# Optimization experiments

Hardware: AMD Instinct MI355X
Metric: run time of the kernel (lower is better)

## Reference

```python
import jax, jax.numpy as jnp
import numpy as np

B, T, C, H, D = 4, 1024, 1024, 16, 64  # batch, seq, n_embd, heads, head_size


def setup_inputs() -> dict:
    key = jax.random.key(0)
    ks = jax.random.split(key, 6)
    x = jax.random.normal(ks[0], (B, T, C), dtype=jnp.float32)
    s = 0.02
    Wq = jax.random.normal(ks[1], (H, C, D), dtype=jnp.float32) * s
    Wk = jax.random.normal(ks[2], (H, C, D), dtype=jnp.float32) * s
    Wv = jax.random.normal(ks[3], (H, C, D), dtype=jnp.float32) * s
    Wo = jax.random.normal(ks[4], (H * D, C), dtype=jnp.float32) * s
    bo = jnp.zeros((C,), dtype=jnp.float32)
    return {"x": x, "Wq": Wq, "Wk": Wk, "Wv": Wv, "Wo": Wo, "bo": bo}


def reference(x, Wq, Wk, Wv, Wo, bo):
    # per-head projections (bias=False Linears), all heads batched via einsum
    q = jnp.einsum("btc,hcd->bhtd", x, Wq)
    k = jnp.einsum("btc,hcd->bhtd", x, Wk)
    v = jnp.einsum("btc,hcd->bhtd", x, Wv)
    # scaled dot-product scores: [B,H,T,T]
    scale = 1.0 / jnp.sqrt(jnp.asarray(D, dtype=q.dtype))
    scores = jnp.einsum("bhtd,bhsd->bhts", q, k) * scale
    # causal mask (tril), masked_fill with -inf equivalent
    causal = jnp.tril(jnp.ones((T, T), dtype=bool))
    neg = jnp.finfo(scores.dtype).min
    scores = jnp.where(causal[None, None], scores, neg)
    att = jax.nn.softmax(scores, axis=-1)
    # weighted aggregation of values, then concat heads
    out = jnp.einsum("bhts,bhsd->bhtd", att, v)
    out = out.transpose(0, 2, 1, 3).reshape(B, T, H * D)
    # output projection
    return out @ Wo + bo
```

## Files before the change

### kernel.cpp

```cpp
#include <hip/hip_runtime.h>
#include <hip/hip_bf16.h>
#include <stdint.h>


typedef float f32x4 __attribute__((ext_vector_type(4)));
typedef __bf16 bf16x8 __attribute__((ext_vector_type(8)));
typedef __bf16 bf16x4 __attribute__((ext_vector_type(4)));

#define GAS __attribute__((address_space(1)))
#define LAS __attribute__((address_space(3)))

__global__ __launch_bounds__(256) void cast_bf16_kernel(
    const float* __restrict__ in, __bf16* __restrict__ out, int n4) {
  int i = blockIdx.x * 256 + threadIdx.x;
  if (i < n4) {
    float4 f = ((const float4*)in)[i];
    bf16x4 o;
    o[0] = (__bf16)f.x; o[1] = (__bf16)f.y; o[2] = (__bf16)f.z; o[3] = (__bf16)f.w;
    ((bf16x4*)out)[i] = o;
  }
}

__global__ __launch_bounds__(256) void transpose_qkv_kernel(
    const float* __restrict__ Wq, const float* __restrict__ Wk,
    const float* __restrict__ Wv, __bf16* __restrict__ dst_base) {
  __shared__ float tile[64][65];
  int z = blockIdx.z;
  const float* s = (z < 16 ? Wq : (z < 32 ? Wk : Wv)) + (size_t)(z & 15) * 65536;
  __bf16* d = dst_base + (size_t)z * 65536;
  int r0 = blockIdx.x * 64;
  int tx = threadIdx.x & 63, ty = threadIdx.x >> 6;
#pragma unroll
  for (int rr = ty; rr < 64; rr += 4)
    tile[rr][tx] = s[(size_t)(r0 + rr) * 64 + tx];
  __syncthreads();
#pragma unroll
  for (int rr = ty; rr < 64; rr += 4)
    d[(size_t)rr * 1024 + (r0 + tx)] = (__bf16)tile[tx][rr];
}

__global__ __launch_bounds__(256) void transpose_cast_kernel(
    const float* __restrict__ src, __bf16* __restrict__ dst,
    int src_ld, int dst_ld) {
  __shared__ float tile[64][65];
  int r0 = blockIdx.x * 64, c0 = blockIdx.y * 64;
  int tx = threadIdx.x & 63, ty = threadIdx.x >> 6;
#pragma unroll
  for (int rr = ty; rr < 64; rr += 4)
    tile[rr][tx] = src[(size_t)(r0 + rr) * src_ld + (c0 + tx)];
  __syncthreads();
#pragma unroll
  for (int rr = ty; rr < 64; rr += 4)
    dst[(size_t)(c0 + rr) * dst_ld + (r0 + tx)] = (__bf16)tile[tx][rr];
}

template <int MODE>
__global__ __launch_bounds__(256) void gemm_bt_kernel(
    const __bf16* __restrict__ A, const __bf16* __restrict__ BT, int N,
    __bf16* __restrict__ qo, __bf16* __restrict__ ko, __bf16* __restrict__ vo,
    float* __restrict__ Cout, const float* __restrict__ bias) {
  constexpr int K = 1024;
  extern __shared__ __align__(16) char smem_raw[];
  __bf16* Ash = (__bf16*)smem_raw;
  __bf16* Bsh = Ash + 2 * 128 * 32;
  const int tid = threadIdx.x;
  const int wid = tid >> 6, lane = tid & 63;
  const int fr = lane & 15, fq = lane >> 4;
  const int m0 = blockIdx.x * 128, n0 = blockIdx.y * 128;
  const int wr = wid >> 1, wc = wid & 1;
  const int srow = lane >> 2;
  const int scol = (((lane & 3) ^ ((lane >> 3) & 3))) * 8;
  const int swz = ((fq ^ ((fr >> 1) & 3))) << 3;

  f32x4 acc[4][4] = {};

  auto stage = [&](int k0, int buf) {
#pragma unroll
    for (int i = 0; i < 2; ++i) {
      int chunk = wid * 2 + i;
      int row = chunk * 16 + srow;
      const __bf16* gA = A + (size_t)(m0 + row) * K + k0 + scol;
      const __bf16* gB = BT + (size_t)(n0 + row) * K + k0 + scol;
      __builtin_amdgcn_global_load_lds((const GAS void*)gA, (LAS void*)&Ash[buf * 4096 + chunk * 512], 16, 0, 0);
      __builtin_amdgcn_global_load_lds((const GAS void*)gB, (LAS void*)&Bsh[buf * 4096 + chunk * 512], 16, 0, 0);
    }
  };

  stage(0, 0);
  __syncthreads();
  int buf = 0;
  for (int k0 = 0; k0 < K; k0 += 32) {
    if (k0 + 32 < K) stage(k0 + 32, buf ^ 1);
    bf16x8 af[4], bfr[4];
#pragma unroll
    for (int mi = 0; mi < 4; ++mi) {
      int r = wr * 64 + mi * 16 + fr;
      af[mi] = *(const bf16x8*)&Ash[buf * 4096 + r * 32 + swz];
    }
#pragma unroll
    for (int ni = 0; ni < 4; ++ni) {
      int r = wc * 64 + ni * 16 + fr;
      bfr[ni] = *(const bf16x8*)&Bsh[buf * 4096 + r * 32 + swz];
    }
    __builtin_amdgcn_s_setprio(1);
#pragma unroll
    for (int mi = 0; mi < 4; ++mi)
#pragma unroll
      for (int ni = 0; ni < 4; ++ni)
        acc[mi][ni] = __builtin_amdgcn_mfma_f32_16x16x32_bf16(af[mi], bfr[ni], acc[mi][ni], 0, 0, 0);
    __builtin_amdgcn_s_setprio(0);
    __syncthreads();
    buf ^= 1;
  }

  if (MODE == 0 && (n0 >> 10) == 2) {
    __bf16* spill = (__bf16*)smem_raw;
#pragma unroll
    for (int mi = 0; mi < 4; ++mi)
#pragma unroll
      for (int ni = 0; ni < 4; ++ni) {
        int nl = wc * 64 + ni * 16 + fr;
        int ml = wr * 64 + mi * 16 + fq * 4;
        bf16x4 pk;
#pragma unroll
        for (int r = 0; r < 4; ++r) pk[r] = (__bf16)acc[mi][ni][r];
        *(bf16x4*)&spill[nl * 136 + ml] = pk;
      }
    __syncthreads();
    const int b = m0 >> 10, t0 = m0 & 1023;
    const int lrow = lane >> 4, lch = lane & 15;
#pragma unroll
    for (int i = 0; i < 8; ++i) {
      int nl = wid * 32 + i * 4 + lrow;
      bf16x8 v = *(const bf16x8*)&spill[nl * 136 + lch * 8];
      int nn = (n0 & 1023) + nl;
      *(bf16x8*)&vo[(((size_t)b * 16 + (nn >> 6)) * 64 + (nn & 63)) * 1024 + t0 + lch * 8] = v;
    }
    return;
  }

#pragma unroll
  for (int mi = 0; mi < 4; ++mi) {
#pragma unroll
    for (int ni = 0; ni < 4; ++ni) {
      int n = n0 + wc * 64 + ni * 16 + fr;
      int mb = m0 + wr * 64 + mi * 16 + fq * 4;
#pragma unroll
      for (int r = 0; r < 4; ++r) {
        int m = mb + r;
        float val = acc[mi][ni][r];
        if (MODE == 0) {
          int sec = n >> 10, nl = n & 1023;
          int h = nl >> 6, dd = nl & 63;
          int b = m >> 10, t = m & 1023;
          if (sec == 0) {
            qo[(((size_t)b * 16 + h) * 1024 + t) * 64 + dd] = (__bf16)(val * 0.125f);
          } else {
            ko[(((size_t)b * 16 + h) * 1024 + t) * 64 + dd] = (__bf16)val;
          }
        } else {
          Cout[(size_t)m * N + n] = val + bias[n];
        }
      }
    }
  }
}

__global__ __launch_bounds__(256) void attn_fwd_kernel(
    const __bf16* __restrict__ Q, const __bf16* __restrict__ Kg,
    const __bf16* __restrict__ Vt, __bf16* __restrict__ O) {
  __shared__ __align__(16) __bf16 Ksh[2][64 * 64];
  __shared__ __align__(16) __bf16 VTs[2][64 * 64];
  __shared__ __align__(16) __bf16 Psh[4][16 * 72];

  const int bid = blockIdx.x;
  const int bx = (bid >> 3) & 7;
  const int bh = (bid & 7) | ((bid >> 6) << 3);
  const int b = bh >> 4, h = bh & 15;
  const size_t base = (size_t)bh * 1024 * 64;
  const int tid = threadIdx.x, wid = tid >> 6, lane = tid & 63;
  const int fr = lane & 15, fq = lane >> 4;
  const int qta = bx, qtb = 15 - bx;
  const int q0a = qta * 64, q0b = qtb * 64;

  bf16x8 qa[2], qbf[2];
  {
    int qra = q0a + wid * 16 + fr;
    qa[0] = *(const bf16x8*)&Q[base + (size_t)qra * 64 + fq * 8];
    qa[1] = *(const bf16x8*)&Q[base + (size_t)qra * 64 + 32 + fq * 8];
    int qrb = q0b + wid * 16 + fr;
    qbf[0] = *(const bf16x8*)&Q[base + (size_t)qrb * 64 + fq * 8];
    qbf[1] = *(const bf16x8*)&Q[base + (size_t)qrb * 64 + 32 + fq * 8];
  }
  f32x4 oa[4] = {}, ob[4] = {};
  float ma = -1e30f, la = 0.f, mb = -1e30f, lb = 0.f;

  const int lrow8 = lane >> 3;
  const int schunk = (lane & 7) ^ lrow8;

  auto stage = [&](int st, int buf) {
    const int s0 = st * 64;
#pragma unroll
    for (int i = 0; i < 2; ++i) {
      int rowbase = i * 32 + wid * 8;
      int row = rowbase + lrow8;
      const __bf16* gK = Kg + base + (size_t)(s0 + row) * 64 + schunk * 8;
      __builtin_amdgcn_global_load_lds((const GAS void*)gK,
          (LAS void*)&Ksh[buf][rowbase * 64], 16, 0, 0);
      const __bf16* gV = Vt + base + (size_t)row * 1024 + s0 + schunk * 8;
      __builtin_amdgcn_global_load_lds((const GAS void*)gV,
          (LAS void*)&VTs[buf][rowbase * 64], 16, 0, 0);
    }
  };

  auto compute = [&](int buf, int s0, const bf16x8* qf, f32x4* oacc,
                     float& m, float& l, int q0x, bool maskT) {
    f32x4 s[4];
    __builtin_amdgcn_s_setprio(1);
#pragma unroll
    for (int sf = 0; sf < 4; ++sf) {
      int row = sf * 16 + fr, rx = fr & 7;
      bf16x8 kf0 = *(const bf16x8*)&Ksh[buf][row * 64 + ((fq ^ rx) << 3)];
      f32x4 z = {};
      s[sf] = __builtin_amdgcn_mfma_f32_16x16x32_bf16(kf0, qf[0], z, 0, 0, 0);
      bf16x8 kf1 = *(const bf16x8*)&Ksh[buf][row * 64 + (((4 + fq) ^ rx) << 3)];
      s[sf] = __builtin_amdgcn_mfma_f32_16x16x32_bf16(kf1, qf[1], s[sf], 0, 0, 0);
    }
    __builtin_amdgcn_s_setprio(0);

    const int qg = q0x + wid * 16 + fr;
    float sv[4][4];
    float mx = -1e30f;
#pragma unroll
    for (int sf = 0; sf < 4; ++sf)
#pragma unroll
      for (int r = 0; r < 4; ++r) {
        float x = s[sf][r];
        if (maskT) { int sg = s0 + sf * 16 + fq * 4 + r; if (sg > qg) x = -1e30f; }
        sv[sf][r] = x;
        mx = fmaxf(mx, x);
      }
    mx = fmaxf(mx, __shfl_xor(mx, 16));
    mx = fmaxf(mx, __shfl_xor(mx, 32));
    float mnew = fmaxf(m, mx);
    float alpha = __expf(m - mnew);
    m = mnew;
    float rs = 0.f;
#pragma unroll
    for (int sf = 0; sf < 4; ++sf) {
      bf16x4 pk;
#pragma unroll
      for (int r = 0; r < 4; ++r) {
        float p = __expf(sv[sf][r] - mnew);
        rs += p;
        pk[r] = (__bf16)p;
      }
      *(bf16x4*)&Psh[wid][fr * 72 + sf * 16 + fq * 4] = pk;
    }
    rs += __shfl_xor(rs, 16);
    rs += __shfl_xor(rs, 32);
    l = l * alpha + rs;
    float ar[4];
#pragma unroll
    for (int r = 0; r < 4; ++r) ar[r] = __shfl(alpha, (lane & 48) | (fq * 4 + r));
#pragma unroll
    for (int df = 0; df < 4; ++df)
#pragma unroll
      for (int r = 0; r < 4; ++r) oacc[df][r] *= ar[r];

    __builtin_amdgcn_s_setprio(1);
#pragma unroll
    for (int kk = 0; kk < 2; ++kk) {
      bf16x8 pf = *(const bf16x8*)&Psh[wid][fr * 72 + kk * 32 + fq * 8];
#pragma unroll
      for (int df = 0; df < 4; ++df) {
        int row = df * 16 + fr;
        bf16x8 vf = *(const bf16x8*)&VTs[buf][row * 64 + ((((kk << 2) | fq) ^ (fr & 7)) << 3)];
        oacc[df] = __builtin_amdgcn_mfma_f32_16x16x32_bf16(pf, vf, oacc[df], 0, 0, 0);
      }
    }
    __builtin_amdgcn_s_setprio(0);
  };

  stage(0, 0);
  __syncthreads();
  int cur = 0;
  for (int st = 0; st <= qtb; ++st) {
    if (st < qtb) stage(st + 1, cur ^ 1);
    compute(cur, st * 64, qbf, ob, mb, lb, q0b, st == qtb);
    if (st <= qta) compute(cur, st * 64, qa, oa, ma, la, q0a, st == qta);
    __syncthreads();
    cur ^= 1;
  }

  auto epilogue = [&](const f32x4* oacc, float l, int q0x) {
    float lr[4];
#pragma unroll
    for (int r = 0; r < 4; ++r) lr[r] = __shfl(l, (lane & 48) | (fq * 4 + r));
#pragma unroll
    for (int r = 0; r < 4; ++r) {
      float inv = 1.0f / lr[r];
      int t = q0x + wid * 16 + fq * 4 + r;
      size_t orow = ((size_t)b * 1024 + t) * 1024 + h * 64;
#pragma unroll
      for (int df = 0; df < 4; ++df)
        O[orow + df * 16 + fr] = (__bf16)(oacc[df][r] * inv);
    }
  };
  epilogue(ob, lb, q0b);
  epilogue(oa, la, q0a);
}

extern "C" void kernel_launch(void* const* d_in, const int* in_sizes, int n_in,
                              void* d_out, int out_size, void* d_ws, size_t ws_size,
                              hipStream_t stream) {
  const float* x  = (const float*)d_in[0];
  const float* Wq = (const float*)d_in[1];
  const float* Wk = (const float*)d_in[2];
  const float* Wv = (const float*)d_in[3];
  const float* Wo = (const float*)d_in[4];
  const float* bo = (const float*)d_in[5];
  float* out = (float*)d_out;

  __bf16* xb    = (__bf16*)d_ws;
  __bf16* wqkvT = xb + (size_t)4096 * 1024;
  __bf16* woT   = wqkvT + (size_t)3072 * 1024;
  __bf16* qb    = woT + (size_t)1024 * 1024;
  __bf16* kb    = qb + (size_t)4 * 16 * 1024 * 64;
  __bf16* vtb   = kb + (size_t)4 * 16 * 1024 * 64;
  __bf16* Ob    = vtb + (size_t)4 * 16 * 1024 * 64;

  cast_bf16_kernel<<<4096, 256, 0, stream>>>(x, xb, 4194304 / 4);
  transpose_qkv_kernel<<<dim3(16, 1, 48), 256, 0, stream>>>(Wq, Wk, Wv, wqkvT);
  transpose_cast_kernel<<<dim3(16, 16), 256, 0, stream>>>(Wo, woT, 1024, 1024);

  gemm_bt_kernel<0><<<dim3(32, 24), 256, 34816, stream>>>(xb, wqkvT, 3072, qb, kb, vtb, nullptr, nullptr);

  attn_fwd_kernel<<<512, 256, 0, stream>>>(qb, kb, vtb, Ob);

  gemm_bt_kernel<1><<<dim3(32, 8), 256, 32768, stream>>>(Ob, woT, 1024, nullptr, nullptr, nullptr, out, bo);
}
```

Measured before the change: 102.3 us.

## Split paired causal q-tiles into separate blocks and add lazy softmax rescaling

The attention kernel no longer pairs a short and a long causal query tile in one block. It launches 1024 blocks of one q-tile each, ordered longest-first, to double parallelism and let the scheduler balance the work. It also skips the running-max update and accumulator rescale unless some lane's new max exceeds the old one by more than 8, which removes exp, shuffle and multiply work on most iterations. Each block reloads its K/V tiles without sharing them between two q-tiles, and the lazy threshold lets exponentials grow up to e^8 before they are renormalized, which stays within fp32/bf16 range.

```diff
diff --git a/kernel.cpp b/kernel.cpp
--- a/kernel.cpp
+++ b/kernel.cpp
@@ -150,10 +150,10 @@
         int m = mb + r;
         float val = acc[mi][ni][r];
         if (MODE == 0) {
-          int sec = n >> 10, nl = n & 1023;
+          int nl = n & 1023;
           int h = nl >> 6, dd = nl & 63;
           int b = m >> 10, t = m & 1023;
-          if (sec == 0) {
+          if ((n >> 10) == 0) {
             qo[(((size_t)b * 16 + h) * 1024 + t) * 64 + dd] = (__bf16)(val * 0.125f);
           } else {
             ko[(((size_t)b * 16 + h) * 1024 + t) * 64 + dd] = (__bf16)val;
@@ -174,26 +174,22 @@
   __shared__ __align__(16) __bf16 Psh[4][16 * 72];
 
   const int bid = blockIdx.x;
-  const int bx = (bid >> 3) & 7;
-  const int bh = (bid & 7) | ((bid >> 6) << 3);
+  const int qt = 15 - (bid >> 6);
+  const int bh = bid & 63;
   const int b = bh >> 4, h = bh & 15;
   const size_t base = (size_t)bh * 1024 * 64;
   const int tid = threadIdx.x, wid = tid >> 6, lane = tid & 63;
   const int fr = lane & 15, fq = lane >> 4;
-  const int qta = bx, qtb = 15 - bx;
-  const int q0a = qta * 64, q0b = qtb * 64;
-
-  bf16x8 qa[2], qbf[2];
+  const int q0 = qt * 64;
+
+  bf16x8 qf[2];
   {
-    int qra = q0a + wid * 16 + fr;
-    qa[0] = *(const bf16x8*)&Q[base + (size_t)qra * 64 + fq * 8];
-    qa[1] = *(const bf16x8*)&Q[base + (size_t)qra * 64 + 32 + fq * 8];
-    int qrb = q0b + wid * 16 + fr;
-    qbf[0] = *(const bf16x8*)&Q[base + (size_t)qrb * 64 + fq * 8];
-    qbf[1] = *(const bf16x8*)&Q[base + (size_t)qrb * 64 + 32 + fq * 8];
-  }
-  f32x4 oa[4] = {}, ob[4] = {};
-  float ma = -1e30f, la = 0.f, mb = -1e30f, lb = 0.f;
+    int qr = q0 + wid * 16 + fr;
+    qf[0] = *(const bf16x8*)&Q[base + (size_t)qr * 64 + fq * 8];
+    qf[1] = *(const bf16x8*)&Q[base + (size_t)qr * 64 + 32 + fq * 8];
+  }
+  f32x4 oacc[4] = {};
+  float m = -1e30f, l = 0.f;
 
   const int lrow8 = lane >> 3;
   const int schunk = (lane & 7) ^ lrow8;
@@ -213,8 +209,7 @@
     }
   };
 
-  auto compute = [&](int buf, int s0, const bf16x8* qf, f32x4* oacc,
-                     float& m, float& l, int q0x, bool maskT) {
+  auto compute = [&](int buf, int s0, bool maskT) {
     f32x4 s[4];
     __builtin_amdgcn_s_setprio(1);
 #pragma unroll
@@ -228,7 +223,7 @@
     }
     __builtin_amdgcn_s_setprio(0);
 
-    const int qg = q0x + wid * 16 + fr;
+    const int qg = q0 + wid * 16 + fr;
     float sv[4][4];
     float mx = -1e30f;
 #pragma unroll
@@ -242,16 +237,26 @@
       }
     mx = fmaxf(mx, __shfl_xor(mx, 16));
     mx = fmaxf(mx, __shfl_xor(mx, 32));
-    float mnew = fmaxf(m, mx);
-    float alpha = __expf(m - mnew);
-    m = mnew;
+    if (__any(mx - m > 8.0f)) {
+      float mnew = fmaxf(m, mx);
+      float alpha = __expf(m - mnew);
+      m = mnew;
+      l *= alpha;
+      float ar[4];
+#pragma unroll
+      for (int r = 0; r < 4; ++r) ar[r] = __shfl(alpha, (lane & 48) | (fq * 4 + r));
+#pragma unroll
+      for (int df = 0; df < 4; ++df)
+#pragma unroll
+        for (int r = 0; r < 4; ++r) oacc[df][r] *= ar[r];
+    }
     float rs = 0.f;
 #pragma unroll
     for (int sf = 0; sf < 4; ++sf) {
       bf16x4 pk;
 #pragma unroll
       for (int r = 0; r < 4; ++r) {
-        float p = __expf(sv[sf][r] - mnew);
+        float p = __expf(sv[sf][r] - m);
         rs += p;
         pk[r] = (__bf16)p;
       }
@@ -259,14 +264,7 @@
     }
     rs += __shfl_xor(rs, 16);
     rs += __shfl_xor(rs, 32);
-    l = l * alpha + rs;
-    float ar[4];
-#pragma unroll
-    for (int r = 0; r < 4; ++r) ar[r] = __shfl(alpha, (lane & 48) | (fq * 4 + r));
-#pragma unroll
-    for (int df = 0; df < 4; ++df)
-#pragma unroll
-      for (int r = 0; r < 4; ++r) oacc[df][r] *= ar[r];
+    l += rs;
 
     __builtin_amdgcn_s_setprio(1);
 #pragma unroll
@@ -285,30 +283,25 @@
   stage(0, 0);
   __syncthreads();
   int cur = 0;
-  for (int st = 0; st <= qtb; ++st) {
-    if (st < qtb) stage(st + 1, cur ^ 1);
-    compute(cur, st * 64, qbf, ob, mb, lb, q0b, st == qtb);
-    if (st <= qta) compute(cur, st * 64, qa, oa, ma, la, q0a, st == qta);
+  for (int st = 0; st <= qt; ++st) {
+    if (st < qt) stage(st + 1, cur ^ 1);
+    compute(cur, st * 64, st == qt);
     __syncthreads();
     cur ^= 1;
   }
 
-  auto epilogue = [&](const f32x4* oacc, float l, int q0x) {
-    float lr[4];
-#pragma unroll
-    for (int r = 0; r < 4; ++r) lr[r] = __shfl(l, (lane & 48) | (fq * 4 + r));
-#pragma unroll
-    for (int r = 0; r < 4; ++r) {
-      float inv = 1.0f / lr[r];
-      int t = q0x + wid * 16 + fq * 4 + r;
-      size_t orow = ((size_t)b * 1024 + t) * 1024 + h * 64;
-#pragma unroll
-      for (int df = 0; df < 4; ++df)
-        O[orow + df * 16 + fr] = (__bf16)(oacc[df][r] * inv);
-    }
-  };
-  epilogue(ob, lb, q0b);
-  epilogue(oa, la, q0a);
+  float lr[4];
+#pragma unroll
+  for (int r = 0; r < 4; ++r) lr[r] = __shfl(l, (lane & 48) | (fq * 4 + r));
+#pragma unroll
+  for (int r = 0; r < 4; ++r) {
+    float inv = 1.0f / lr[r];
+    int t = q0 + wid * 16 + fq * 4 + r;
+    size_t orow = ((size_t)b * 1024 + t) * 1024 + h * 64;
+#pragma unroll
+    for (int df = 0; df < 4; ++df)
+      O[orow + df * 16 + fr] = (__bf16)(oacc[df][r] * inv);
+  }
 }
 
 extern "C" void kernel_launch(void* const* d_in, const int* in_sizes, int n_in,
@@ -336,7 +329,8 @@
 
   gemm_bt_kernel<0><<<dim3(32, 24), 256, 34816, stream>>>(xb, wqkvT, 3072, qb, kb, vtb, nullptr, nullptr);
 
-  attn_fwd_kernel<<<512, 256, 0, stream>>>(qb, kb, vtb, Ob);
-
-  gemm_bt_kernel<1><<<dim3(32, 8), 256, 32768, stream>>>(Ob, woT, 1024, nullptr, nullptr, nullptr, out, bo);
-}
+  attn_fwd_kernel<<<1024, 256, 0, stream>>>(qb, kb, vtb, Ob);
+
+  gemm_bt_kernel<1><<<dim3(32, 8), 256, 32768, stream>>>(Ob, woT, 1024,
+      nullptr, nullptr, nullptr, out, bo);
+}
```

Result: faster. 95.27 us (-6.9%).
